# Optimization experiments

Hardware: AMD Instinct MI355X
Metric: run time of the kernel (lower is better)

Reference implementation:

```python
import jax, jax.numpy as jnp
import numpy as np

# pywt db2 decomposition filters (len 4)
_DEC_LO = np.array([-0.12940952255126037, 0.22414386804201339, 0.8365163037378079, 0.48296291314453416], dtype=np.float32)
_DEC_HI = np.array([-0.48296291314453416, 0.8365163037378079, -0.22414386804201339, -0.12940952255126037], dtype=np.float32)


def _dwt1d(x, filt, axis):
    # pywt-style single-level DWT along `axis`, mode='symmetric'.
    x = jnp.moveaxis(x, axis, -1)
    L = x.shape[-1]
    flen = filt.shape[0]
    pad = [(0, 0)] * (x.ndim - 1) + [(flen - 1, flen - 1)]
    ext = jnp.pad(x, pad, mode='symmetric')            # (..., L + 2*flen - 2)
    outlen = (L + flen - 1) // 2
    fr = filt[::-1]
    out = None
    for k in range(flen):  # tiny fixed loop over 4 taps
        tap = jax.lax.slice_in_dim(ext, 1 + k, 1 + k + 2 * outlen, 2, axis=-1)
        out = fr[k] * tap if out is None else out + fr[k] * tap
    return jnp.moveaxis(out, -1, axis)


def _dwt2(x):
    lo = jnp.asarray(_DEC_LO)
    hi = jnp.asarray(_DEC_HI)
    lo_w = _dwt1d(x, lo, -1)
    cA = _dwt1d(lo_w, lo, -2)   # approx-approx
    cH = _dwt1d(lo_w, hi, -2)   # detail along H, approx along W (pywt cH)
    return cA, cH


def setup_inputs() -> dict:
    key = jax.random.key(0)
    ks = jax.random.split(key, 4)
    B, C, H, W = 8, 128, 256, 256
    hidden = C // 11  # reduction = 11
    x = jax.random.normal(ks[0], (B, C, H, W), dtype=jnp.float32)
    w1 = jax.random.normal(ks[1], (C, hidden), dtype=jnp.float32) * 0.05
    b1 = jnp.zeros((hidden,), dtype=jnp.float32)
    w2 = jax.random.normal(ks[2], (hidden, C), dtype=jnp.float32) * 0.05
    b2 = jnp.zeros((C,), dtype=jnp.float32)
    w_sa = jax.random.normal(ks[3], (1, 2, 5, 5), dtype=jnp.float32) * 0.05
    return {"x": x, "w1": w1, "b1": b1, "w2": w2, "b2": b2, "w_sa": w_sa}


def reference(x, w1, b1, w2, b2, w_sa):
    B, C, H, W = x.shape
    cA, cH = _dwt2(x)                                   # [B,C,Hc,Wc]
    # channel attention: avg-pool(cA) + max-pool(cH) -> MLP -> sigmoid
    avg_pool = jnp.mean(cA, axis=(2, 3))                # [B,C]
    max_pool = jnp.max(cH, axis=(2, 3))                 # [B,C]
    p = avg_pool + max_pool
    h = jax.nn.relu(p @ w1 + b1)
    channel_att = jax.nn.sigmoid(h @ w2 + b2)           # [B,C]
    channel_att = channel_att[:, :, None, None]
    # spatial attention on concat(cA, cH) over channels
    sp = jnp.concatenate([cA, cH], axis=1)              # [B,2C,Hc,Wc]
    avg_out = jnp.mean(sp, axis=1, keepdims=True)
    max_out = jnp.max(sp, axis=1, keepdims=True)
    sa_in = jnp.concatenate([avg_out, max_out], axis=1) # [B,2,Hc,Wc]
    sa = jax.lax.conv_general_dilated(
        sa_in, w_sa, window_strides=(1, 1), padding=[(2, 2), (2, 2)],
        dimension_numbers=("NCHW", "OIHW", "NCHW"))     # [B,1,Hc,Wc]
    sa = jax.nn.sigmoid(sa)
    # upsample the half-resolution spatial map back to (H, W) to gate x
    sa = jax.image.resize(sa, (B, 1, H, W), method="bilinear")
    return x * channel_att * sa
```

## Files before the change

### kernel.cpp

```cpp
#include <hip/hip_runtime.h>
#include <math.h>

#define B_N 8
#define C_CH 128
#define H_IN 256
#define W_IN 256
#define HO 129
#define WO 129
#define SP (HO*WO)
#define HIDDEN 11
#define NSTR 16
#define SH 8
#define NGE 32
#define CPW 4
#define WOP 132

__constant__ float c_lo[4] = {-0.12940952255126037f, 0.2241438680420134f,
                               0.8365163037378079f,  0.48296291314453416f};
__constant__ float c_hi[4] = {-0.48296291314453416f, 0.8365163037378079f,
                              -0.2241438680420134f, -0.12940952255126037f};

struct CS {
  float4 cur0, cur1, nxt0, nxt1;
  float w00, w01, w02;
  float w10, w11, w12;
  float w20, w21, w22;
  float w30, w31, w32;
  float sA, mH;
};

__global__ __launch_bounds__(256) void dwt_stream_kernel(
    const float* __restrict__ x,
    float* __restrict__ psum, float* __restrict__ pmax,
    float* __restrict__ chpsum, float* __restrict__ chpmax)
{
  const int bid  = blockIdx.x;
  const int s    = bid & (NSTR - 1);
  const int gb   = (bid >> 4) & 7;
  const int b    = bid >> 7;
  const int tid  = threadIdx.x;
  const int lane = tid & 63;
  const int wave = tid >> 6;
  const int g    = gb * 4 + wave;
  const int cb   = g * CPW;
  const int j0   = s * SH;

  const float lo0 = c_lo[0], lo1 = c_lo[1], lo2 = c_lo[2], lo3 = c_lo[3];
  const float hi0 = c_hi[0], hi1 = c_hi[1], hi2 = c_hi[2], hi3 = c_hi[3];
  const float l03 = lo0 + lo3, l12 = lo1 + lo2;
  const float h03 = hi0 + hi3, h12 = hi1 + hi2;

  const float* xb0 = x + ((size_t)(b * C_CH + cb) + 0) * (H_IN * W_IN) + 4 * lane;
  const float* xb1 = xb0 + (H_IN * W_IN);
  const float* xb2 = xb1 + (H_IN * W_IN);
  const float* xb3 = xb2 + (H_IN * W_IN);

  CS s0, s1, s2, s3;
#define INIT(S) do { \
    S.w00=0.f;S.w01=0.f;S.w02=0.f; S.w10=0.f;S.w11=0.f;S.w12=0.f; \
    S.w20=0.f;S.w21=0.f;S.w22=0.f; S.w30=0.f;S.w31=0.f;S.w32=0.f; \
    S.sA=0.f; S.mH=-INFINITY; } while(0)
  INIT(s0); INIT(s1); INIT(s2); INIT(s3);

  float* cps = chpsum + ((size_t)(b * NGE + g)) * (HO * WOP);
  float* cpm = chpmax + ((size_t)(b * NGE + g)) * (HO * WOP);

#define LOADC(S, XB, R) do { \
    const float* _p = (XB) + (R) * W_IN; \
    S.cur0 = *reinterpret_cast<const float4*>(_p); \
    S.cur1 = *reinterpret_cast<const float4*>(_p + W_IN); } while(0)

#define LOADN(S, XB, R) do { \
    const float* _p = (XB) + (R) * W_IN; \
    S.nxt0 = *reinterpret_cast<const float4*>(_p); \
    S.nxt1 = *reinterpret_cast<const float4*>(_p + W_IN); } while(0)

#define SWAPB(S) do { S.cur0 = S.nxt0; S.cur1 = S.nxt1; } while(0)

#define HROW(S, V) do { \
    float _pz = __shfl_up((V).z, 1); \
    float _pw = __shfl_up((V).w, 1); \
    float _l0 = (lane == 0) ? (l03 * (V).y + l12 * (V).x) \
                            : (lo0*(V).y + lo1*(V).x + lo2*_pw + lo3*_pz); \
    float _l1 = lo0*(V).w + lo1*(V).z + lo2*(V).y + lo3*(V).x; \
    float _l2 = l03 * (V).z + l12 * (V).w; \
    S.w00=S.w10; S.w10=S.w20; S.w20=S.w30; S.w30=_l0; \
    S.w01=S.w11; S.w11=S.w21; S.w21=S.w31; S.w31=_l1; \
    S.w02=S.w12; S.w12=S.w22; S.w22=S.w32; S.w32=_l2; } while(0)

#define EMITN(S) do { \
    float _a0 = lo0*S.w30 + lo1*S.w20 + lo2*S.w10 + lo3*S.w00; \
    float _h0 = hi0*S.w30 + hi1*S.w20 + hi2*S.w10 + hi3*S.w00; \
    float _a1 = lo0*S.w31 + lo1*S.w21 + lo2*S.w11 + lo3*S.w01; \
    float _h1 = hi0*S.w31 + hi1*S.w21 + hi2*S.w11 + hi3*S.w01; \
    float _a2 = lo0*S.w32 + lo1*S.w22 + lo2*S.w12 + lo3*S.w02; \
    float _h2 = hi0*S.w32 + hi1*S.w22 + hi2*S.w12 + hi3*S.w02; \
    S.sA += _a0 + _a1; S.mH = fmaxf(S.mH, fmaxf(_h0, _h1)); \
    if (lane == 63) { S.sA += _a2; S.mH = fmaxf(S.mH, _h2); } \
    cs0 += _a0 + _h0; cs1 += _a1 + _h1; cs2 += _a2 + _h2; \
    cm0 = fmaxf(cm0, fmaxf(_a0, _h0)); \
    cm1 = fmaxf(cm1, fmaxf(_a1, _h1)); \
    cm2 = fmaxf(cm2, fmaxf(_a2, _h2)); } while(0)

#define EMITT(S) do { \
    float _a0 = l03*S.w30 + l12*S.w20; float _h0 = h03*S.w30 + h12*S.w20; \
    float _a1 = l03*S.w31 + l12*S.w21; float _h1 = h03*S.w31 + h12*S.w21; \
    float _a2 = l03*S.w32 + l12*S.w22; float _h2 = h03*S.w32 + h12*S.w22; \
    S.sA += _a0 + _a1; S.mH = fmaxf(S.mH, fmaxf(_h0, _h1)); \
    if (lane == 63) { S.sA += _a2; S.mH = fmaxf(S.mH, _h2); } \
    cs0 += _a0 + _h0; cs1 += _a1 + _h1; cs2 += _a2 + _h2; \
    cm0 = fmaxf(cm0, fmaxf(_a0, _h0)); \
    cm1 = fmaxf(cm1, fmaxf(_a1, _h1)); \
    cm2 = fmaxf(cm2, fmaxf(_a2, _h2)); } while(0)

#define EMITB(S) do { \
    float _a0 = l03*S.w20 + l12*S.w30; float _h0 = h03*S.w20 + h12*S.w30; \
    float _a1 = l03*S.w21 + l12*S.w31; float _h1 = h03*S.w21 + h12*S.w31; \
    float _a2 = l03*S.w22 + l12*S.w32; float _h2 = h03*S.w22 + h12*S.w32; \
    S.sA += _a0 + _a1; S.mH = fmaxf(S.mH, fmaxf(_h0, _h1)); \
    if (lane == 63) { S.sA += _a2; S.mH = fmaxf(S.mH, _h2); } \
    cs0 += _a0 + _h0; cs1 += _a1 + _h1; cs2 += _a2 + _h2; \
    cm0 = fmaxf(cm0, fmaxf(_a0, _h0)); \
    cm1 = fmaxf(cm1, fmaxf(_a1, _h1)); \
    cm2 = fmaxf(cm2, fmaxf(_a2, _h2)); } while(0)

#define STORE_CROSS(JO) do { \
    float* _ps = cps + (size_t)(JO) * WOP; \
    float* _pm = cpm + (size_t)(JO) * WOP; \
    *reinterpret_cast<float2*>(_ps + 2 * lane) = make_float2(cs0, cs1); \
    *reinterpret_cast<float2*>(_pm + 2 * lane) = make_float2(cm0, cm1); \
    if (lane == 63) { _ps[128] = cs2; _pm[128] = cm2; } } while(0)

  const int rstart = (s == 0) ? 0 : (2 * j0 - 2);
  const int npairs = (s == 0) ? SH : (SH + 1);

  LOADC(s0, xb0, rstart); LOADC(s1, xb1, rstart);
  LOADC(s2, xb2, rstart); LOADC(s3, xb3, rstart);

  for (int p = 0; p < npairs; ++p) {
    const bool last = (p + 1 == npairs);
    if (!last) {
      const int rn = rstart + 2 * (p + 1);
      LOADN(s0, xb0, rn); LOADN(s1, xb1, rn);
      LOADN(s2, xb2, rn); LOADN(s3, xb3, rn);
    }

    HROW(s0, s0.cur0); HROW(s0, s0.cur1);
    HROW(s1, s1.cur0); HROW(s1, s1.cur1);
    HROW(s2, s2.cur0); HROW(s2, s2.cur1);
    HROW(s3, s3.cur0); HROW(s3, s3.cur1);

    if (s == 0 || p > 0) {
      float cs0 = 0.f, cs1 = 0.f, cs2 = 0.f;
      float cm0 = -INFINITY, cm1 = -INFINITY, cm2 = -INFINITY;
      int jo;
      if (s == 0 && p == 0) {
        EMITT(s0); EMITT(s1); EMITT(s2); EMITT(s3);
        jo = 0;
      } else {
        EMITN(s0); EMITN(s1); EMITN(s2); EMITN(s3);
        jo = (s == 0) ? p : (j0 + p - 1);
      }
      STORE_CROSS(jo);
    }

    if (!last) { SWAPB(s0); SWAPB(s1); SWAPB(s2); SWAPB(s3); }
  }

  if (s == NSTR - 1) {
    float cs0 = 0.f, cs1 = 0.f, cs2 = 0.f;
    float cm0 = -INFINITY, cm1 = -INFINITY, cm2 = -INFINITY;
    EMITB(s0); EMITB(s1); EMITB(s2); EMITB(s3);
    STORE_CROSS(128);
  }

#define REDUCE_CH(S, CH) do { \
    float _ss = S.sA, _sm = S.mH; \
    for (int off = 32; off > 0; off >>= 1) { \
      _ss += __shfl_down(_ss, off, 64); \
      _sm = fmaxf(_sm, __shfl_down(_sm, off, 64)); \
    } \
    if (lane == 0) { \
      size_t _bc = (size_t)(b * C_CH + cb + (CH)); \
      psum[_bc * NSTR + s] = _ss; \
      pmax[_bc * NSTR + s] = _sm; \
    } } while(0)

  REDUCE_CH(s0, 0); REDUCE_CH(s1, 1); REDUCE_CH(s2, 2); REDUCE_CH(s3, 3);
}

__global__ __launch_bounds__(256) void combine_kernel(
    const float* __restrict__ chpsum, const float* __restrict__ chpmax,
    float* __restrict__ sa_in)
{
  int b = blockIdx.y;
  int s = blockIdx.x * 256 + threadIdx.x;
  if (s >= SP) return;
  int jo  = s / WO;
  int col = s - jo * WO;
  size_t off = (size_t)jo * WOP + col;
  float sum = 0.f, mx = -INFINITY;
  #pragma unroll 4
  for (int gg = 0; gg < NGE; ++gg) {
    sum += chpsum[((size_t)(b * NGE + gg)) * (HO * WOP) + off];
    mx = fmaxf(mx, chpmax[((size_t)(b * NGE + gg)) * (HO * WOP) + off]);
  }
  sa_in[(size_t)b * 2 * SP + s]      = sum * (1.f / 256.f);
  sa_in[(size_t)b * 2 * SP + SP + s] = mx;
}

__global__ __launch_bounds__(128) void mlp_kernel(
    const float* __restrict__ psum, const float* __restrict__ pmax,
    const float* __restrict__ w1, const float* __restrict__ b1,
    const float* __restrict__ w2, const float* __restrict__ b2,
    float* __restrict__ att)
{
  int b = blockIdx.x;
  int c = threadIdx.x;
  __shared__ float p[C_CH];
  __shared__ float h[HIDDEN];

  float s = 0.f, m = -INFINITY;
  #pragma unroll
  for (int k = 0; k < NSTR; ++k) {
    s += psum[(b * C_CH + c) * NSTR + k];
    m = fmaxf(m, pmax[(b * C_CH + c) * NSTR + k]);
  }
  p[c] = s * (1.f / 16641.f) + m;
  __syncthreads();

  if (c < HIDDEN) {
    float acc = b1[c];
    for (int k = 0; k < C_CH; ++k) acc += p[k] * w1[k * HIDDEN + c];
    h[c] = fmaxf(acc, 0.f);
  }
  __syncthreads();

  float acc = b2[c];
  #pragma unroll
  for (int j = 0; j < HIDDEN; ++j) acc += h[j] * w2[j * C_CH + c];
  att[b * C_CH + c] = 1.f / (1.f + expf(-acc));
}

__global__ __launch_bounds__(256) void conv_kernel(
    const float* __restrict__ sa_in, const float* __restrict__ w_sa,
    float* __restrict__ sa)
{
  int b = blockIdx.y;
  int s = blockIdx.x * 256 + threadIdx.x;
  if (s >= SP) return;
  int i = s / WO;
  int j = s - i * WO;
  float acc = 0.f;
  const float* in0 = sa_in + (size_t)b * 2 * SP;
  #pragma unroll
  for (int ch = 0; ch < 2; ++ch) {
    const float* in = in0 + ch * SP;
    #pragma unroll
    for (int u = 0; u < 5; ++u) {
      int ii = i + u - 2;
      if (ii < 0 || ii >= HO) continue;
      #pragma unroll
      for (int v = 0; v < 5; ++v) {
        int jj = j + v - 2;
        if (jj < 0 || jj >= WO) continue;
        acc += in[ii * WO + jj] * w_sa[(ch * 5 + u) * 5 + v];
      }
    }
  }
  sa[(size_t)b * SP + s] = 1.f / (1.f + expf(-acc));
}

__global__ __launch_bounds__(256) void resize_kernel(
    const float* __restrict__ sa, float* __restrict__ sar)
{
  int idx = blockIdx.x * 256 + threadIdx.x;
  int J = idx & 255;
  int I = (idx >> 8) & 255;
  int b = idx >> 16;

  float ti = (I + 0.5f) * (129.f / 256.f) - 0.5f;
  ti = fminf(fmaxf(ti, 0.f), 128.f);
  int i0 = (int)ti;
  float fi = ti - (float)i0;
  int i1 = min(i0 + 1, 128);

  float tj = (J + 0.5f) * (129.f / 256.f) - 0.5f;
  tj = fminf(fmaxf(tj, 0.f), 128.f);
  int jj0 = (int)tj;
  float fj = tj - (float)jj0;
  int jj1 = min(jj0 + 1, 128);

  const float* r0 = sa + ((size_t)b * HO + i0) * WO;
  const float* r1 = sa + ((size_t)b * HO + i1) * WO;
  float v0 = r0[jj0] + fj * (r0[jj1] - r0[jj0]);
  float v1 = r1[jj0] + fj * (r1[jj1] - r1[jj0]);
  sar[idx] = v0 + fi * (v1 - v0);
}

__global__ __launch_bounds__(256) void final2_kernel(
    const float* __restrict__ x, const float* __restrict__ att,
    const float* __restrict__ sar, float* __restrict__ out)
{
  int bid = blockIdx.x;
  int cchunk = bid & 3;
  int rg  = (bid >> 2) & 63;
  int b   = bid >> 8;
  int t = threadIdx.x;
  int r = t >> 6;
  int col4 = t & 63;
  int I = rg * 4 + r;

  __shared__ float att_s[32];
  if (t < 32) att_s[t] = att[b * C_CH + cchunk * 32 + t];
  __syncthreads();

  float4 sv = reinterpret_cast<const float4*>(sar + ((size_t)b * 256 + I) * 256)[col4];

  size_t base4 = ((size_t)(b * C_CH + cchunk * 32) * 256 + I) * 64 + col4;
  const float4* xp = reinterpret_cast<const float4*>(x);
  float4* op = reinterpret_cast<float4*>(out);
  #pragma unroll 4
  for (int cc = 0; cc < 32; ++cc) {
    float a = att_s[cc];
    float4 xv = xp[base4 + (size_t)cc * 16384];
    float4 ov;
    ov.x = xv.x * a * sv.x;
    ov.y = xv.y * a * sv.y;
    ov.z = xv.z * a * sv.z;
    ov.w = xv.w * a * sv.w;
    op[base4 + (size_t)cc * 16384] = ov;
  }
}

extern "C" void kernel_launch(void* const* d_in, const int* in_sizes, int n_in,
                              void* d_out, int out_size, void* d_ws, size_t ws_size,
                              hipStream_t stream) {
  const float* x    = (const float*)d_in[0];
  const float* w1   = (const float*)d_in[1];
  const float* b1   = (const float*)d_in[2];
  const float* w2   = (const float*)d_in[3];
  const float* b2   = (const float*)d_in[4];
  const float* w_sa = (const float*)d_in[5];
  float* out = (float*)d_out;

  float* chpsum = (float*)d_ws;
  float* chpmax = chpsum + (size_t)B_N * NGE * HO * WOP;
  float* psum   = chpmax + (size_t)B_N * NGE * HO * WOP;
  float* pmax   = psum + B_N * C_CH * NSTR;
  float* sa_in  = pmax + B_N * C_CH * NSTR;
  float* att    = sa_in + (size_t)B_N * 2 * SP;
  float* sa     = att + B_N * C_CH;
  float* sar    = sa + (size_t)B_N * SP;

  hipLaunchKernelGGL(dwt_stream_kernel, dim3(B_N * 8 * NSTR), dim3(256), 0, stream,
                     x, psum, pmax, chpsum, chpmax);
  hipLaunchKernelGGL(combine_kernel, dim3((SP + 255) / 256, B_N), dim3(256), 0, stream,
                     chpsum, chpmax, sa_in);
  hipLaunchKernelGGL(mlp_kernel, dim3(B_N), dim3(C_CH), 0, stream,
                     psum, pmax, w1, b1, w2, b2, att);
  hipLaunchKernelGGL(conv_kernel, dim3((SP + 255) / 256, B_N), dim3(256), 0, stream,
                     sa_in, w_sa, sa);
  hipLaunchKernelGGL(resize_kernel, dim3(B_N * H_IN * W_IN / 256), dim3(256), 0, stream,
                     sa, sar);
  hipLaunchKernelGGL(final2_kernel, dim3(B_N * 64 * 4), dim3(256), 0, stream,
                     x, att, sar, out);
}
```

Measured before the change: 207.8 us.

## Halve channels per wave in DWT, fuse MLP into combine, resize into final

The DWT streaming kernel now handles 2 channels per wave instead of 4, doubling the number of blocks and adding an occupancy hint so more waves can hide load latency. The price is twice as many cross-channel partial planes for combine to read. The MLP runs as an extra block inside the combine launch, which removes one kernel launch. The bilinear resize is folded into the final gating kernel by staging the needed sa rows in shared memory, which removes the intermediate full-resolution map and its write and read back.

```diff
diff --git a/kernel.cpp b/kernel.cpp
--- a/kernel.cpp
+++ b/kernel.cpp
@@ -11,9 +11,10 @@
 #define HIDDEN 11
 #define NSTR 16
 #define SH 8
-#define NGE 32
-#define CPW 4
+#define NGE 64
+#define CPW 2
 #define WOP 132
+#define NBX 66
 
 __constant__ float c_lo[4] = {-0.12940952255126037f, 0.2241438680420134f,
                                0.8365163037378079f,  0.48296291314453416f};
@@ -29,15 +30,15 @@
   float sA, mH;
 };
 
-__global__ __launch_bounds__(256) void dwt_stream_kernel(
+__global__ __launch_bounds__(256, 4) void dwt_stream_kernel(
     const float* __restrict__ x,
     float* __restrict__ psum, float* __restrict__ pmax,
     float* __restrict__ chpsum, float* __restrict__ chpmax)
 {
   const int bid  = blockIdx.x;
   const int s    = bid & (NSTR - 1);
-  const int gb   = (bid >> 4) & 7;
-  const int b    = bid >> 7;
+  const int gb   = (bid >> 4) & 15;
+  const int b    = bid >> 8;
   const int tid  = threadIdx.x;
   const int lane = tid & 63;
   const int wave = tid >> 6;
@@ -50,17 +51,15 @@
   const float l03 = lo0 + lo3, l12 = lo1 + lo2;
   const float h03 = hi0 + hi3, h12 = hi1 + hi2;
 
-  const float* xb0 = x + ((size_t)(b * C_CH + cb) + 0) * (H_IN * W_IN) + 4 * lane;
+  const float* xb0 = x + ((size_t)(b * C_CH + cb)) * (H_IN * W_IN) + 4 * lane;
   const float* xb1 = xb0 + (H_IN * W_IN);
-  const float* xb2 = xb1 + (H_IN * W_IN);
-  const float* xb3 = xb2 + (H_IN * W_IN);
-
-  CS s0, s1, s2, s3;
+
+  CS s0, s1;
 #define INIT(S) do { \
     S.w00=0.f;S.w01=0.f;S.w02=0.f; S.w10=0.f;S.w11=0.f;S.w12=0.f; \
     S.w20=0.f;S.w21=0.f;S.w22=0.f; S.w30=0.f;S.w31=0.f;S.w32=0.f; \
     S.sA=0.f; S.mH=-INFINITY; } while(0)
-  INIT(s0); INIT(s1); INIT(s2); INIT(s3);
+  INIT(s0); INIT(s1);
 
   float* cps = chpsum + ((size_t)(b * NGE + g)) * (HO * WOP);
   float* cpm = chpmax + ((size_t)(b * NGE + g)) * (HO * WOP);
@@ -135,42 +134,38 @@
   const int npairs = (s == 0) ? SH : (SH + 1);
 
   LOADC(s0, xb0, rstart); LOADC(s1, xb1, rstart);
-  LOADC(s2, xb2, rstart); LOADC(s3, xb3, rstart);
 
   for (int p = 0; p < npairs; ++p) {
     const bool last = (p + 1 == npairs);
     if (!last) {
       const int rn = rstart + 2 * (p + 1);
       LOADN(s0, xb0, rn); LOADN(s1, xb1, rn);
-      LOADN(s2, xb2, rn); LOADN(s3, xb3, rn);
     }
 
     HROW(s0, s0.cur0); HROW(s0, s0.cur1);
     HROW(s1, s1.cur0); HROW(s1, s1.cur1);
-    HROW(s2, s2.cur0); HROW(s2, s2.cur1);
-    HROW(s3, s3.cur0); HROW(s3, s3.cur1);
 
     if (s == 0 || p > 0) {
       float cs0 = 0.f, cs1 = 0.f, cs2 = 0.f;
       float cm0 = -INFINITY, cm1 = -INFINITY, cm2 = -INFINITY;
       int jo;
       if (s == 0 && p == 0) {
-        EMITT(s0); EMITT(s1); EMITT(s2); EMITT(s3);
+        EMITT(s0); EMITT(s1);
         jo = 0;
       } else {
-        EMITN(s0); EMITN(s1); EMITN(s2); EMITN(s3);
+        EMITN(s0); EMITN(s1);
         jo = (s == 0) ? p : (j0 + p - 1);
       }
       STORE_CROSS(jo);
     }
 
-    if (!last) { SWAPB(s0); SWAPB(s1); SWAPB(s2); SWAPB(s3); }
+    if (!last) { SWAPB(s0); SWAPB(s1); }
   }
 
   if (s == NSTR - 1) {
     float cs0 = 0.f, cs1 = 0.f, cs2 = 0.f;
     float cm0 = -INFINITY, cm1 = -INFINITY, cm2 = -INFINITY;
-    EMITB(s0); EMITB(s1); EMITB(s2); EMITB(s3);
+    EMITB(s0); EMITB(s1);
     STORE_CROSS(128);
   }
 
@@ -186,15 +181,51 @@
       pmax[_bc * NSTR + s] = _sm; \
     } } while(0)
 
-  REDUCE_CH(s0, 0); REDUCE_CH(s1, 1); REDUCE_CH(s2, 2); REDUCE_CH(s3, 3);
+  REDUCE_CH(s0, 0); REDUCE_CH(s1, 1);
 }
 
 __global__ __launch_bounds__(256) void combine_kernel(
     const float* __restrict__ chpsum, const float* __restrict__ chpmax,
-    float* __restrict__ sa_in)
+    float* __restrict__ sa_in,
+    const float* __restrict__ psum, const float* __restrict__ pmax,
+    const float* __restrict__ w1, const float* __restrict__ b1,
+    const float* __restrict__ w2, const float* __restrict__ b2,
+    float* __restrict__ att)
 {
   int b = blockIdx.y;
-  int s = blockIdx.x * 256 + threadIdx.x;
+  int bx = blockIdx.x;
+  int t = threadIdx.x;
+
+  if (bx == NBX) {
+    __shared__ float p[C_CH];
+    __shared__ float h[HIDDEN];
+    int c = t;
+    if (c < C_CH) {
+      float s = 0.f, m = -INFINITY;
+      #pragma unroll
+      for (int k = 0; k < NSTR; ++k) {
+        s += psum[(b * C_CH + c) * NSTR + k];
+        m = fmaxf(m, pmax[(b * C_CH + c) * NSTR + k]);
+      }
+      p[c] = s * (1.f / 16641.f) + m;
+    }
+    __syncthreads();
+    if (c < HIDDEN) {
+      float acc = b1[c];
+      for (int k = 0; k < C_CH; ++k) acc += p[k] * w1[k * HIDDEN + c];
+      h[c] = fmaxf(acc, 0.f);
+    }
+    __syncthreads();
+    if (c < C_CH) {
+      float acc = b2[c];
+      #pragma unroll
+      for (int j = 0; j < HIDDEN; ++j) acc += h[j] * w2[j * C_CH + c];
+      att[b * C_CH + c] = 1.f / (1.f + expf(-acc));
+    }
+    return;
+  }
+
+  int s = bx * 256 + t;
   if (s >= SP) return;
   int jo  = s / WO;
   int col = s - jo * WO;
@@ -207,39 +238,6 @@
   }
   sa_in[(size_t)b * 2 * SP + s]      = sum * (1.f / 256.f);
   sa_in[(size_t)b * 2 * SP + SP + s] = mx;
-}
-
-__global__ __launch_bounds__(128) void mlp_kernel(
-    const float* __restrict__ psum, const float* __restrict__ pmax,
-    const float* __restrict__ w1, const float* __restrict__ b1,
-    const float* __restrict__ w2, const float* __restrict__ b2,
-    float* __restrict__ att)
-{
-  int b = blockIdx.x;
-  int c = threadIdx.x;
-  __shared__ float p[C_CH];
-  __shared__ float h[HIDDEN];
-
-  float s = 0.f, m = -INFINITY;
-  #pragma unroll
-  for (int k = 0; k < NSTR; ++k) {
-    s += psum[(b * C_CH + c) * NSTR + k];
-    m = fmaxf(m, pmax[(b * C_CH + c) * NSTR + k]);
-  }
-  p[c] = s * (1.f / 16641.f) + m;
-  __syncthreads();
-
-  if (c < HIDDEN) {
-    float acc = b1[c];
-    for (int k = 0; k < C_CH; ++k) acc += p[k] * w1[k * HIDDEN + c];
-    h[c] = fmaxf(acc, 0.f);
-  }
-  __syncthreads();
-
-  float acc = b2[c];
-  #pragma unroll
-  for (int j = 0; j < HIDDEN; ++j) acc += h[j] * w2[j * C_CH + c];
-  att[b * C_CH + c] = 1.f / (1.f + expf(-acc));
 }
 
 __global__ __launch_bounds__(256) void conv_kernel(
@@ -271,36 +269,9 @@
   sa[(size_t)b * SP + s] = 1.f / (1.f + expf(-acc));
 }
 
-__global__ __launch_bounds__(256) void resize_kernel(
-    const float* __restrict__ sa, float* __restrict__ sar)
-{
-  int idx = blockIdx.x * 256 + threadIdx.x;
-  int J = idx & 255;
-  int I = (idx >> 8) & 255;
-  int b = idx >> 16;
-
-  float ti = (I + 0.5f) * (129.f / 256.f) - 0.5f;
-  ti = fminf(fmaxf(ti, 0.f), 128.f);
-  int i0 = (int)ti;
-  float fi = ti - (float)i0;
-  int i1 = min(i0 + 1, 128);
-
-  float tj = (J + 0.5f) * (129.f / 256.f) - 0.5f;
-  tj = fminf(fmaxf(tj, 0.f), 128.f);
-  int jj0 = (int)tj;
-  float fj = tj - (float)jj0;
-  int jj1 = min(jj0 + 1, 128);
-
-  const float* r0 = sa + ((size_t)b * HO + i0) * WO;
-  const float* r1 = sa + ((size_t)b * HO + i1) * WO;
-  float v0 = r0[jj0] + fj * (r0[jj1] - r0[jj0]);
-  float v1 = r1[jj0] + fj * (r1[jj1] - r1[jj0]);
-  sar[idx] = v0 + fi * (v1 - v0);
-}
-
-__global__ __launch_bounds__(256) void final2_kernel(
+__global__ __launch_bounds__(256) void final3_kernel(
     const float* __restrict__ x, const float* __restrict__ att,
-    const float* __restrict__ sar, float* __restrict__ out)
+    const float* __restrict__ sa, float* __restrict__ out)
 {
   int bid = blockIdx.x;
   int cchunk = bid & 3;
@@ -312,10 +283,39 @@
   int I = rg * 4 + r;
 
   __shared__ float att_s[32];
+  __shared__ float sa_s[4][WOP];
   if (t < 32) att_s[t] = att[b * C_CH + cchunk * 32 + t];
+
+  float ti0 = fminf(fmaxf((rg * 4 + 0.5f) * (129.f / 256.f) - 0.5f, 0.f), 128.f);
+  int ilo = (int)ti0;
+  const float* sab = sa + (size_t)b * SP;
+  if (t < WO) {
+    #pragma unroll
+    for (int rr = 0; rr < 4; ++rr) {
+      int ir = min(ilo + rr, 128);
+      sa_s[rr][t] = sab[ir * WO + t];
+    }
+  }
   __syncthreads();
 
-  float4 sv = reinterpret_cast<const float4*>(sar + ((size_t)b * 256 + I) * 256)[col4];
+  float ti = fminf(fmaxf((I + 0.5f) * (129.f / 256.f) - 0.5f, 0.f), 128.f);
+  int i0 = (int)ti;
+  float fi = ti - (float)i0;
+  int i0r = i0 - ilo;
+  int i1r = min(i0 + 1, 128) - ilo;
+
+  float res[4];
+  #pragma unroll
+  for (int q = 0; q < 4; ++q) {
+    int J = col4 * 4 + q;
+    float tj = fminf(fmaxf((J + 0.5f) * (129.f / 256.f) - 0.5f, 0.f), 128.f);
+    int jj0 = (int)tj;
+    float fj = tj - (float)jj0;
+    int jj1 = min(jj0 + 1, 128);
+    float v0 = sa_s[i0r][jj0] + fj * (sa_s[i0r][jj1] - sa_s[i0r][jj0]);
+    float v1 = sa_s[i1r][jj0] + fj * (sa_s[i1r][jj1] - sa_s[i1r][jj0]);
+    res[q] = v0 + fi * (v1 - v0);
+  }
 
   size_t base4 = ((size_t)(b * C_CH + cchunk * 32) * 256 + I) * 64 + col4;
   const float4* xp = reinterpret_cast<const float4*>(x);
@@ -325,10 +325,10 @@
     float a = att_s[cc];
     float4 xv = xp[base4 + (size_t)cc * 16384];
     float4 ov;
-    ov.x = xv.x * a * sv.x;
-    ov.y = xv.y * a * sv.y;
-    ov.z = xv.z * a * sv.z;
-    ov.w = xv.w * a * sv.w;
+    ov.x = xv.x * a * res[0];
+    ov.y = xv.y * a * res[1];
+    ov.z = xv.z * a * res[2];
+    ov.w = xv.w * a * res[3];
     op[base4 + (size_t)cc * 16384] = ov;
   }
 }
@@ -351,18 +351,13 @@
   float* sa_in  = pmax + B_N * C_CH * NSTR;
   float* att    = sa_in + (size_t)B_N * 2 * SP;
   float* sa     = att + B_N * C_CH;
-  float* sar    = sa + (size_t)B_N * SP;
-
-  hipLaunchKernelGGL(dwt_stream_kernel, dim3(B_N * 8 * NSTR), dim3(256), 0, stream,
+
+  hipLaunchKernelGGL(dwt_stream_kernel, dim3(B_N * 16 * NSTR), dim3(256), 0, stream,
                      x, psum, pmax, chpsum, chpmax);
-  hipLaunchKernelGGL(combine_kernel, dim3((SP + 255) / 256, B_N), dim3(256), 0, stream,
-                     chpsum, chpmax, sa_in);
-  hipLaunchKernelGGL(mlp_kernel, dim3(B_N), dim3(C_CH), 0, stream,
-                     psum, pmax, w1, b1, w2, b2, att);
+  hipLaunchKernelGGL(combine_kernel, dim3(NBX + 1, B_N), dim3(256), 0, stream,
+                     chpsum, chpmax, sa_in, psum, pmax, w1, b1, w2, b2, att);
   hipLaunchKernelGGL(conv_kernel, dim3((SP + 255) / 256, B_N), dim3(256), 0, stream,
                      sa_in, w_sa, sa);
-  hipLaunchKernelGGL(resize_kernel, dim3(B_N * H_IN * W_IN / 256), dim3(256), 0, stream,
-                     sa, sar);
-  hipLaunchKernelGGL(final2_kernel, dim3(B_N * 64 * 4), dim3(256), 0, stream,
-                     x, att, sar, out);
-}
+  hipLaunchKernelGGL(final3_kernel, dim3(B_N * 64 * 4), dim3(256), 0, stream,
+                     x, att, sa, out);
+}
```

Measured after the change: 212.0 us. 1.02x slower.
